# Kernel optimization log

Measured on AMD Instinct MI355X. Metric: run time of the kernel, lower is better.

The kernel has to match this reference:

```python
import jax, jax.numpy as jnp
import numpy as np

N = 65536   # mini-batch of per-element losses
C = 1000    # number of classes (logit dim == super-class id range == weight matrix dims)


def setup_inputs() -> dict:
    key = jax.random.key(0)
    k0, k1, k2, k3 = jax.random.split(key, 4)
    logits = jax.random.normal(k0, (N, C), dtype=jnp.float32)
    target = jax.random.randint(k1, (N,), 0, C, dtype=jnp.int64)
    class_weights = jax.random.uniform(k2, (C, C), dtype=jnp.float32)
    super_classes = jax.random.randint(k3, (C,), 0, C, dtype=jnp.int64)
    return {"logits": logits, "class_weights": class_weights,
            "target": target, "super_classes": super_classes}


def reference(logits, class_weights, target, super_classes):
    # log_softmax over class dim (single stable pass)
    logp = jax.nn.log_softmax(logits, axis=1)                      # [N, C]
    # truetarget = super_classes[target]  (super-class id per sample)
    truetarget = super_classes[target]                             # [N]
    # predicted class per sample
    predtarget = jnp.argmax(logp, axis=1)                          # [N]
    # w2 = class_weights[truetarget].gather(1, predtarget) == class_weights[truetarget, predtarget]
    w = class_weights[truetarget, predtarget]                      # [N]
    # logp.index_select(-1, truetarget).diag() == logp[i, truetarget[i]] — direct gather,
    # no O(N^2) intermediate
    tgt_logp = jnp.take_along_axis(logp, truetarget[:, None], axis=1)[:, 0]  # [N]
    l2 = -w * tgt_logp
    l3 = jnp.sum(l2) / jnp.sum(w)
    return l3
```

## Files before the change

kernel.cpp:

```cpp
#include <hip/hip_runtime.h>
#include <math.h>

#define CCOLS 1000
#define NF4   250
#define RPW   8
#define WPB   4

typedef float f32x4 __attribute__((ext_vector_type(4)));

__device__ __forceinline__ f32x4 ntload(const f32x4* p) {
    return __builtin_nontemporal_load(p);
}

__device__ __forceinline__ void loadrow(f32x4& b0, f32x4& b1, f32x4& b2, f32x4& b3,
                                        const float* __restrict__ logits, int row, int lane) {
    const f32x4* rp = (const f32x4*)(logits + (size_t)row * CCOLS);
    b0 = ntload(rp + lane);
    b1 = ntload(rp + 64 + lane);
    b2 = ntload(rp + 128 + lane);
    if (lane < NF4 - 192) {
        b3 = ntload(rp + 192 + lane);
    } else {
        const f32x4 ninf = {-INFINITY, -INFINITY, -INFINITY, -INFINITY};
        b3 = ninf;
    }
}

__device__ __forceinline__ void process_row(f32x4 v0, f32x4 v1, f32x4 v2, f32x4 v3,
                                            int lane, int tt, float tval,
                                            const float* __restrict__ cw,
                                            float& num, float& den) {
    float m = -INFINITY;
#pragma unroll
    for (int j = 0; j < 4; ++j) {
        m = fmaxf(m, v0[j]); m = fmaxf(m, v1[j]);
        m = fmaxf(m, v2[j]); m = fmaxf(m, v3[j]);
    }
#pragma unroll
    for (int s = 32; s >= 1; s >>= 1) m = fmaxf(m, __shfl_xor(m, s, 64));

    float ssum = 0.0f;
    int   mi   = 0x7fffffff;
#pragma unroll
    for (int j = 0; j < 4; ++j) {
        { const float x = v0[j]; const int c = lane * 4 + j;
          ssum += __expf(x - m); if (x == m) mi = min(mi, c); }
        { const float x = v1[j]; const int c = (64 + lane) * 4 + j;
          ssum += __expf(x - m); if (x == m) mi = min(mi, c); }
        { const float x = v2[j]; const int c = (128 + lane) * 4 + j;
          ssum += __expf(x - m); if (x == m) mi = min(mi, c); }
        { const float x = v3[j]; const int c = (192 + lane) * 4 + j;
          ssum += __expf(x - m); if (x == m) mi = min(mi, c); }
    }
#pragma unroll
    for (int s = 32; s >= 1; s >>= 1) {
        ssum += __shfl_xor(ssum, s, 64);
        mi = min(mi, __shfl_xor(mi, s, 64));
    }

    const float lse = m + __logf(ssum);
    const float w = cw[(size_t)tt * CCOLS + mi];
    num += w * (lse - tval);
    den += w;
}

__global__ __launch_bounds__(256) void cacel_rows_kernel(
    const float* __restrict__ logits,
    const float* __restrict__ cw,
    const int*   __restrict__ tgt,
    const int*   __restrict__ sc,
    float*       __restrict__ partials,
    int nrows)
{
    const int wid  = threadIdx.x >> 6;
    const int lane = threadIdx.x & 63;
    const int W    = blockIdx.x * WPB + wid;
    const int r0   = __builtin_amdgcn_readfirstlane(W * RPW);

    int   tts[RPW];
    float tvals[RPW];
#pragma unroll
    for (int k = 0; k < RPW; ++k) {
        const int row = r0 + k;
        tts[k] = (row < nrows) ? sc[tgt[row]] : 0;
    }
#pragma unroll
    for (int k = 0; k < RPW; ++k) {
        const int row = r0 + k;
        tvals[k] = (row < nrows) ? logits[(size_t)row * CCOLS + tts[k]] : 0.0f;
    }

    float num = 0.0f, den = 0.0f;

    f32x4 a0, a1, a2, a3, b0, b1, b2, b3;
    if (r0 < nrows) loadrow(a0, a1, a2, a3, logits, r0, lane);

#pragma unroll
    for (int k = 0; k < RPW; ++k) {
        const int row = r0 + k;
        if (row < nrows) {
            if ((k & 1) == 0) {
                if (k + 1 < RPW && row + 1 < nrows)
                    loadrow(b0, b1, b2, b3, logits, row + 1, lane);
                process_row(a0, a1, a2, a3, lane, tts[k], tvals[k], cw, num, den);
            } else {
                if (k + 1 < RPW && row + 1 < nrows)
                    loadrow(a0, a1, a2, a3, logits, row + 1, lane);
                process_row(b0, b1, b2, b3, lane, tts[k], tvals[k], cw, num, den);
            }
        }
    }

    __shared__ float snum[WPB], sden[WPB];
    if (lane == 0) { snum[wid] = num; sden[wid] = den; }
    __syncthreads();
    if (threadIdx.x == 0) {
        partials[2 * (size_t)blockIdx.x + 0] = snum[0] + snum[1] + snum[2] + snum[3];
        partials[2 * (size_t)blockIdx.x + 1] = sden[0] + sden[1] + sden[2] + sden[3];
    }
}

__global__ __launch_bounds__(256) void cacel_final_kernel(
    const float* __restrict__ partials, int nblk, float* __restrict__ out)
{
    float n = 0.0f, d = 0.0f;
    for (int i = threadIdx.x; i < nblk; i += 256) {
        n += partials[2 * (size_t)i + 0];
        d += partials[2 * (size_t)i + 1];
    }
    __shared__ float sn[256], sd[256];
    sn[threadIdx.x] = n;
    sd[threadIdx.x] = d;
    __syncthreads();
    for (int s = 128; s > 0; s >>= 1) {
        if (threadIdx.x < s) {
            sn[threadIdx.x] += sn[threadIdx.x + s];
            sd[threadIdx.x] += sd[threadIdx.x + s];
        }
        __syncthreads();
    }
    if (threadIdx.x == 0) out[0] = sn[0] / sd[0];
}

extern "C" void kernel_launch(void* const* d_in, const int* in_sizes, int n_in,
                              void* d_out, int out_size, void* d_ws, size_t ws_size,
                              hipStream_t stream) {
    (void)n_in; (void)out_size; (void)ws_size;
    const float* logits = (const float*)d_in[0];
    const float* cw     = (const float*)d_in[1];
    const int*   tgt    = (const int*)d_in[2];
    const int*   sc     = (const int*)d_in[3];

    const int N    = in_sizes[2];
    const int rows_per_block = WPB * RPW;
    const int nblk = (N + rows_per_block - 1) / rows_per_block;

    float* partials = (float*)d_ws;

    cacel_rows_kernel<<<nblk, 256, 0, stream>>>(logits, cw, tgt, sc, partials, N);
    cacel_final_kernel<<<1, 256, 0, stream>>>(partials, nblk, (float*)d_out);
}
```

Baseline: 56.66 us.

## Fuse final reduction via fixed-point atomics and last-block finalize

Replaces the separate single-block reduction kernel with 64-bit fixed-point atomic accumulation of per-block numerator and denominator, plus a ticket counter so the last block computes the final ratio. It also moves wave-uniform values (super-class ids, target logits, argmax index) into scalar registers and sets an occupancy hint in launch bounds. The goal is to remove the second launch and its serial tail, at the cost of a memset, atomic contention, and quantization to 2^-32 resolution, which truncates negative partial sums incorrectly.

```diff
diff --git a/kernel.cpp b/kernel.cpp
--- a/kernel.cpp
+++ b/kernel.cpp
@@ -12,17 +12,21 @@
     return __builtin_nontemporal_load(p);
 }
 
-__device__ __forceinline__ void loadrow(f32x4& b0, f32x4& b1, f32x4& b2, f32x4& b3,
-                                        const float* __restrict__ logits, int row, int lane) {
-    const f32x4* rp = (const f32x4*)(logits + (size_t)row * CCOLS);
-    b0 = ntload(rp + lane);
-    b1 = ntload(rp + 64 + lane);
-    b2 = ntload(rp + 128 + lane);
+__device__ __forceinline__ float sgpr_f32(float x) {
+    return __int_as_float(__builtin_amdgcn_readfirstlane(__float_as_int(x)));
+}
+
+__device__ __forceinline__ void loadrow(f32x4& v0, f32x4& v1, f32x4& v2, f32x4& v3,
+                                        const float* __restrict__ rowbase, int lane) {
+    const f32x4* rp = (const f32x4*)rowbase;
+    v0 = ntload(rp + lane);
+    v1 = ntload(rp + lane + 64);
+    v2 = ntload(rp + lane + 128);
     if (lane < NF4 - 192) {
-        b3 = ntload(rp + 192 + lane);
+        v3 = ntload(rp + lane + 192);
     } else {
         const f32x4 ninf = {-INFINITY, -INFINITY, -INFINITY, -INFINITY};
-        b3 = ninf;
+        v3 = ninf;
     }
 }
 
@@ -59,41 +63,42 @@
     }
 
     const float lse = m + __logf(ssum);
-    const float w = cw[(size_t)tt * CCOLS + mi];
+    const int mis = __builtin_amdgcn_readfirstlane(mi);
+    const float w = cw[(size_t)tt * CCOLS + mis];
     num += w * (lse - tval);
     den += w;
 }
 
-__global__ __launch_bounds__(256) void cacel_rows_kernel(
+__global__ __launch_bounds__(256, 8) void cacel_kernel(
     const float* __restrict__ logits,
     const float* __restrict__ cw,
     const int*   __restrict__ tgt,
     const int*   __restrict__ sc,
-    float*       __restrict__ partials,
+    unsigned long long* __restrict__ acc,
+    float*       __restrict__ out,
     int nrows)
 {
     const int wid  = threadIdx.x >> 6;
     const int lane = threadIdx.x & 63;
-    const int W    = blockIdx.x * WPB + wid;
-    const int r0   = __builtin_amdgcn_readfirstlane(W * RPW);
+    const int r0   = __builtin_amdgcn_readfirstlane((blockIdx.x * WPB + wid) * RPW);
 
     int   tts[RPW];
     float tvals[RPW];
 #pragma unroll
     for (int k = 0; k < RPW; ++k) {
         const int row = r0 + k;
-        tts[k] = (row < nrows) ? sc[tgt[row]] : 0;
+        tts[k] = (row < nrows) ? __builtin_amdgcn_readfirstlane(sc[tgt[row]]) : 0;
     }
 #pragma unroll
     for (int k = 0; k < RPW; ++k) {
         const int row = r0 + k;
-        tvals[k] = (row < nrows) ? logits[(size_t)row * CCOLS + tts[k]] : 0.0f;
+        tvals[k] = (row < nrows) ? sgpr_f32(logits[(size_t)row * CCOLS + tts[k]]) : 0.0f;
     }
 
     float num = 0.0f, den = 0.0f;
 
     f32x4 a0, a1, a2, a3, b0, b1, b2, b3;
-    if (r0 < nrows) loadrow(a0, a1, a2, a3, logits, r0, lane);
+    if (r0 < nrows) loadrow(a0, a1, a2, a3, logits + (size_t)r0 * CCOLS, lane);
 
 #pragma unroll
     for (int k = 0; k < RPW; ++k) {
@@ -101,11 +106,11 @@
         if (row < nrows) {
             if ((k & 1) == 0) {
                 if (k + 1 < RPW && row + 1 < nrows)
-                    loadrow(b0, b1, b2, b3, logits, row + 1, lane);
+                    loadrow(b0, b1, b2, b3, logits + (size_t)(row + 1) * CCOLS, lane);
                 process_row(a0, a1, a2, a3, lane, tts[k], tvals[k], cw, num, den);
             } else {
                 if (k + 1 < RPW && row + 1 < nrows)
-                    loadrow(a0, a1, a2, a3, logits, row + 1, lane);
+                    loadrow(a0, a1, a2, a3, logits + (size_t)(row + 1) * CCOLS, lane);
                 process_row(b0, b1, b2, b3, lane, tts[k], tvals[k], cw, num, den);
             }
         }
@@ -115,31 +120,23 @@
     if (lane == 0) { snum[wid] = num; sden[wid] = den; }
     __syncthreads();
     if (threadIdx.x == 0) {
-        partials[2 * (size_t)blockIdx.x + 0] = snum[0] + snum[1] + snum[2] + snum[3];
-        partials[2 * (size_t)blockIdx.x + 1] = sden[0] + sden[1] + sden[2] + sden[3];
+        const double SCALE = 4294967296.0;
+        const double bn = (double)snum[0] + snum[1] + snum[2] + snum[3];
+        const double bd = (double)sden[0] + sden[1] + sden[2] + sden[3];
+        const unsigned long long qn = (unsigned long long)(bn * SCALE);
+        const unsigned long long qd = (unsigned long long)(bd * SCALE);
+        __hip_atomic_fetch_add(&acc[0], qn, __ATOMIC_RELAXED, __HIP_MEMORY_SCOPE_AGENT);
+        __hip_atomic_fetch_add(&acc[1], qd, __ATOMIC_RELAXED, __HIP_MEMORY_SCOPE_AGENT);
+        const unsigned int t = __hip_atomic_fetch_add(
+            (unsigned int*)&acc[2], 1u, __ATOMIC_ACQ_REL, __HIP_MEMORY_SCOPE_AGENT);
+        if (t == gridDim.x - 1) {
+            const unsigned long long n64 =
+                __hip_atomic_load(&acc[0], __ATOMIC_RELAXED, __HIP_MEMORY_SCOPE_AGENT);
+            const unsigned long long d64 =
+                __hip_atomic_load(&acc[1], __ATOMIC_RELAXED, __HIP_MEMORY_SCOPE_AGENT);
+            out[0] = (float)((double)n64 / (double)d64);
+        }
     }
-}
-
-__global__ __launch_bounds__(256) void cacel_final_kernel(
-    const float* __restrict__ partials, int nblk, float* __restrict__ out)
-{
-    float n = 0.0f, d = 0.0f;
-    for (int i = threadIdx.x; i < nblk; i += 256) {
-        n += partials[2 * (size_t)i + 0];
-        d += partials[2 * (size_t)i + 1];
-    }
-    __shared__ float sn[256], sd[256];
-    sn[threadIdx.x] = n;
-    sd[threadIdx.x] = d;
-    __syncthreads();
-    for (int s = 128; s > 0; s >>= 1) {
-        if (threadIdx.x < s) {
-            sn[threadIdx.x] += sn[threadIdx.x + s];
-            sd[threadIdx.x] += sd[threadIdx.x + s];
-        }
-        __syncthreads();
-    }
-    if (threadIdx.x == 0) out[0] = sn[0] / sd[0];
 }
 
 extern "C" void kernel_launch(void* const* d_in, const int* in_sizes, int n_in,
@@ -155,8 +152,8 @@
     const int rows_per_block = WPB * RPW;
     const int nblk = (N + rows_per_block - 1) / rows_per_block;
 
-    float* partials = (float*)d_ws;
+    unsigned long long* acc = (unsigned long long*)d_ws;
 
-    cacel_rows_kernel<<<nblk, 256, 0, stream>>>(logits, cw, tgt, sc, partials, N);
-    cacel_final_kernel<<<1, 256, 0, stream>>>(partials, nblk, (float*)d_out);
+    hipMemsetAsync(d_ws, 0, 3 * sizeof(unsigned long long), stream);
+    cacel_kernel<<<nblk, 256, 0, stream>>>(logits, cw, tgt, sc, acc, (float*)d_out, N);
 }
```

Result: slower. 154.6 us (+172.9%).
